# Performance work log

Measured on AMD Instinct MI355X. Metric: run time of the kernel, lower is better.

## Reference

```python
import jax, jax.numpy as jnp
import numpy as np

N_HEAD = 16


def setup_inputs() -> dict:
    B, T, C, H = 64, 128, 2048, N_HEAD
    hd = C // H
    key = jax.random.key(0)
    ks = jax.random.split(key, 5)
    x = jax.random.normal(ks[0], (B, T, C), dtype=jnp.float32)
    wq = jax.random.normal(ks[1], (C, C), dtype=jnp.float32) * 0.02
    wk = jax.random.normal(ks[2], (C, C), dtype=jnp.float32) * 0.02
    wv = jax.random.normal(ks[3], (C, C), dtype=jnp.float32) * 0.02
    wo = jax.random.normal(ks[4], (C, C), dtype=jnp.float32) * 0.02
    # RoPE frequencies: freqs_cis = exp(i * pos * theta_j), theta_j = 10000^(-2j/hd)
    pos = jnp.arange(T, dtype=jnp.float32)
    inv_freq = 1.0 / (10000.0 ** (jnp.arange(0, hd, 2, dtype=jnp.float32) / hd))  # [hd/2]
    ang = pos[:, None] * inv_freq[None, :]  # [T, hd/2]
    return {
        "x": x,
        "freqs_cos": jnp.cos(ang),
        "freqs_sin": jnp.sin(ang),
        "wq": wq, "wk": wk, "wv": wv, "wo": wo,
    }


def _apply_rope(t, cos, sin):
    # t: [B,T,H,hd]; complex multiply on interleaved (even, odd) pairs
    B, T, H, hd = t.shape
    tr = t.reshape(B, T, H, hd // 2, 2)
    te, to = tr[..., 0], tr[..., 1]
    c = cos[None, :, None, :]  # [1,T,1,hd/2]
    s = sin[None, :, None, :]
    oe = te * c - to * s
    oo = te * s + to * c
    return jnp.stack([oe, oo], axis=-1).reshape(B, T, H, hd)


def reference(x, freqs_cos, freqs_sin, wq, wk, wv, wo):
    B, T, C = x.shape
    H = N_HEAD
    hd = C // H
    q = (x @ wq.T).reshape(B, T, H, hd)
    k = (x @ wk.T).reshape(B, T, H, hd)
    v = (x @ wv.T).reshape(B, T, H, hd)
    q = _apply_rope(q, freqs_cos, freqs_sin)
    k = _apply_rope(k, freqs_cos, freqs_sin)
    # scores: [B,H,T,S]
    scores = jnp.einsum("bthd,bshd->bhts", q, k) / (hd ** 0.5)
    causal = jnp.tril(jnp.ones((T, T), dtype=bool))
    scores = jnp.where(causal[None, None], scores, jnp.float32(-jnp.inf))
    probs = jax.nn.softmax(scores, axis=-1)  # dropout is identity in eval
    out = jnp.einsum("bhts,bshd->bthd", probs, v).reshape(B, T, C)
    return out @ wo.T
```

## Files before the change

kernel.cpp:

```cpp
#include <hip/hip_runtime.h>
#include <cstdint>


typedef unsigned short ushort;
typedef __bf16 bf16x8 __attribute__((ext_vector_type(8)));
typedef float floatx4 __attribute__((ext_vector_type(4)));

__device__ __forceinline__ ushort f2bf(float f) {
  union { float f; uint32_t u; } v; v.f = f;
  uint32_t r = v.u + 0x7FFFu + ((v.u >> 16) & 1u);
  return (ushort)(r >> 16);
}
__device__ __forceinline__ float bf2f(ushort h) {
  union { uint32_t u; float f; } v; v.u = ((uint32_t)h) << 16;
  return v.f;
}

__device__ __forceinline__ void load_lds16(const void* g, void* l) {
  __builtin_amdgcn_global_load_lds(
      (__attribute__((address_space(1))) void*)(uintptr_t)g,
      (__attribute__((address_space(3))) void*)(uint32_t)(uintptr_t)l,
      16, 0, 0);
}

__device__ __forceinline__ void store_out(ushort* C, size_t i, float v) { C[i] = f2bf(v); }
__device__ __forceinline__ void store_out(float* C, size_t i, float v) { C[i] = v; }

template <typename OutT>
__device__ __forceinline__ void gemm_bt_body(const ushort* __restrict__ A,
                                             const ushort* __restrict__ B,
                                             OutT* __restrict__ C,
                                             int M, int N, int K) {
  __shared__ __align__(16) ushort As[128 * 32];
  __shared__ __align__(16) ushort Bs[128 * 32];
  const int tid = threadIdx.x;
  const int wave = tid >> 6, lane = tid & 63;
  const int quad = lane >> 4, colv = lane & 15;
  const int m0 = blockIdx.x * 128, n0 = blockIdx.y * 128;
  const int wm = (wave & 1) * 64, wn = (wave >> 1) * 64;

  floatx4 acc[4][4] = {};

  const int row0 = tid >> 2;
  const int gsw = (tid & 3) ^ ((row0 >> 1) & 3);
  const int c0 = gsw * 8;

  int aoff[4], boff[4];
#pragma unroll
  for (int i = 0; i < 4; ++i) {
    int ra = wm + i * 16 + colv;
    aoff[i] = ra * 32 + ((quad ^ ((ra >> 1) & 3)) << 3);
    int rb = wn + i * 16 + colv;
    boff[i] = rb * 32 + ((quad ^ ((rb >> 1) & 3)) << 3);
  }

  for (int k0 = 0; k0 < K; k0 += 32) {
    if (k0) __syncthreads();
    const ushort* Ab = A + (size_t)(m0 + row0) * K + k0 + c0;
    const ushort* Bb = B + (size_t)(n0 + row0) * K + k0 + c0;
    load_lds16(Ab, &As[wave * 512]);
    load_lds16(Bb, &Bs[wave * 512]);
    load_lds16(Ab + (size_t)64 * K, &As[wave * 512 + 2048]);
    load_lds16(Bb + (size_t)64 * K, &Bs[wave * 512 + 2048]);
    __syncthreads();

    bf16x8 af[4], bfr[4];
#pragma unroll
    for (int i = 0; i < 4; ++i) af[i] = *(const bf16x8*)&As[aoff[i]];
#pragma unroll
    for (int j = 0; j < 4; ++j) bfr[j] = *(const bf16x8*)&Bs[boff[j]];
#pragma unroll
    for (int i = 0; i < 4; ++i)
#pragma unroll
      for (int j = 0; j < 4; ++j)
        acc[i][j] = __builtin_amdgcn_mfma_f32_16x16x32_bf16(af[i], bfr[j], acc[i][j], 0, 0, 0);
  }

#pragma unroll
  for (int i = 0; i < 4; ++i)
#pragma unroll
    for (int j = 0; j < 4; ++j)
#pragma unroll
      for (int r = 0; r < 4; ++r) {
        int m = m0 + wm + i * 16 + quad * 4 + r;
        int n = n0 + wn + j * 16 + colv;
        store_out(C, (size_t)m * N + n, acc[i][j][r]);
      }
}

__global__ __launch_bounds__(256) void gemm_qkv(
    const ushort* __restrict__ A, const ushort* __restrict__ Wq,
    const ushort* __restrict__ Wk, const ushort* __restrict__ Wv,
    ushort* __restrict__ Q, ushort* __restrict__ Kb, ushort* __restrict__ V) {
  const ushort* B = (blockIdx.z == 0) ? Wq : (blockIdx.z == 1) ? Wk : Wv;
  ushort* C = (blockIdx.z == 0) ? Q : (blockIdx.z == 1) ? Kb : V;
  gemm_bt_body<ushort>(A, B, C, 8192, 2048, 2048);
}

__global__ __launch_bounds__(256) void gemm_out_k(
    const ushort* __restrict__ A, const ushort* __restrict__ B,
    float* __restrict__ C) {
  gemm_bt_body<float>(A, B, C, 8192, 2048, 2048);
}

#define NX 4194304u
#define NW 1048576u
__global__ void cvt_all(const float* __restrict__ x, const float* __restrict__ wq,
                        const float* __restrict__ wk, const float* __restrict__ wv,
                        const float* __restrict__ wo,
                        ushort* __restrict__ xb, ushort* __restrict__ wqb,
                        ushort* __restrict__ wkb, ushort* __restrict__ wvb,
                        ushort* __restrict__ wob) {
  uint32_t i = blockIdx.x * 256u + threadIdx.x;
  const float* src;
  ushort* dst;
  uint32_t off;
  if (i < NX) {
    src = x; dst = xb; off = i;
  } else {
    uint32_t i2 = i - NX;
    uint32_t r = i2 >> 20;
    off = i2 & (NW - 1u);
    src = (r == 0) ? wq : (r == 1) ? wk : (r == 2) ? wv : wo;
    dst = (r == 0) ? wqb : (r == 1) ? wkb : (r == 2) ? wvb : wob;
  }
  float4 v = ((const float4*)src)[off];
  ushort4 o;
  o.x = f2bf(v.x); o.y = f2bf(v.y); o.z = f2bf(v.z); o.w = f2bf(v.w);
  ((ushort4*)dst)[off] = o;
}

__global__ __launch_bounds__(256) void attn_kernel(
    const ushort* __restrict__ Q, const ushort* __restrict__ K,
    const ushort* __restrict__ V, const float* __restrict__ Cf,
    const float* __restrict__ Sf, ushort* __restrict__ O) {
  __shared__ __align__(16) ushort Qs[128 * 128];
  __shared__ __align__(16) ushort KVs[128 * 128];
  const int b = blockIdx.x >> 4, h = blockIdx.x & 15;
  const int tid = threadIdx.x, wave = tid >> 6, lane = tid & 63;
  const int quad = lane >> 4, colv = lane & 15;
  const size_t gbase = (size_t)b * 262144 + (size_t)h * 128;

#pragma unroll
  for (int sgi = 0; sgi < 8; ++sgi) {
    int seg = tid + sgi * 256;
    int t = seg >> 4, g = seg & 15;
    uint4 qv = *(const uint4*)(Q + gbase + (size_t)t * 2048 + g * 8);
    uint4 kv = *(const uint4*)(K + gbase + (size_t)t * 2048 + g * 8);
    float4 cf = *(const float4*)(Cf + t * 64 + g * 4);
    float4 sf = *(const float4*)(Sf + t * 64 + g * 4);
    uint32_t* qw = (uint32_t*)&qv;
    uint32_t* kw = (uint32_t*)&kv;
#pragma unroll
    for (int j = 0; j < 4; ++j) {
      float c = (&cf.x)[j], s = (&sf.x)[j];
      uint32_t w = qw[j];
      float e = bf2f((ushort)(w & 0xFFFF)), o = bf2f((ushort)(w >> 16));
      qw[j] = (uint32_t)f2bf(e * c - o * s) | ((uint32_t)f2bf(e * s + o * c) << 16);
      w = kw[j];
      e = bf2f((ushort)(w & 0xFFFF)); o = bf2f((ushort)(w >> 16));
      kw[j] = (uint32_t)f2bf(e * c - o * s) | ((uint32_t)f2bf(e * s + o * c) << 16);
    }
    int so = t * 128 + ((g ^ (t & 15)) << 3);
    *(uint4*)&Qs[so] = qv;
    *(uint4*)&KVs[so] = kv;
  }
  __syncthreads();

  floatx4 accs[2][8] = {};
#pragma unroll
  for (int kc = 0; kc < 4; ++kc) {
    bf16x8 af[2], bfr[8];
#pragma unroll
    for (int i = 0; i < 2; ++i) {
      int r = wave * 32 + i * 16 + colv;
      af[i] = *(const bf16x8*)&Qs[r * 128 + ((((kc << 2) | quad) ^ (r & 15)) << 3)];
    }
#pragma unroll
    for (int j = 0; j < 8; ++j) {
      int r = j * 16 + colv;
      bfr[j] = *(const bf16x8*)&KVs[r * 128 + ((((kc << 2) | quad) ^ (r & 15)) << 3)];
    }
#pragma unroll
    for (int i = 0; i < 2; ++i)
#pragma unroll
      for (int j = 0; j < 8; ++j)
        accs[i][j] = __builtin_amdgcn_mfma_f32_16x16x32_bf16(af[i], bfr[j], accs[i][j], 0, 0, 0);
  }

  const float scale = 0.08838834764831845f;
#pragma unroll
  for (int i = 0; i < 2; ++i)
#pragma unroll
    for (int r = 0; r < 4; ++r) {
      int t = wave * 32 + i * 16 + quad * 4 + r;
      float mx = -1e30f;
#pragma unroll
      for (int j = 0; j < 8; ++j) {
        int s = j * 16 + colv;
        float v = accs[i][j][r] * scale;
        v = (s <= t) ? v : -1e30f;
        accs[i][j][r] = v;
        mx = fmaxf(mx, v);
      }
#pragma unroll
      for (int off = 1; off < 16; off <<= 1) mx = fmaxf(mx, __shfl_xor(mx, off, 64));
      float l = 0.f;
#pragma unroll
      for (int j = 0; j < 8; ++j) {
        float p = __expf(accs[i][j][r] - mx);
        accs[i][j][r] = p;
        l += p;
      }
#pragma unroll
      for (int off = 1; off < 16; off <<= 1) l += __shfl_xor(l, off, 64);
      float inv = 1.0f / l;
#pragma unroll
      for (int j = 0; j < 8; ++j) {
        int s = j * 16 + colv;
        Qs[t * 128 + ((((s >> 3) ^ (t & 15)) << 3) | (s & 7))] = f2bf(accs[i][j][r] * inv);
      }
    }
  __syncthreads();

#pragma unroll
  for (int sgi = 0; sgi < 8; ++sgi) {
    int seg = tid + sgi * 256;
    int t = seg >> 4;
    int dg = (seg & 15) << 3;
    uint4 vv = *(const uint4*)(V + gbase + (size_t)t * 2048 + dg);
    const ushort* vp = (const ushort*)&vv;
#pragma unroll
    for (int jj = 0; jj < 8; ++jj) {
      int d = dg + jj;
      KVs[d * 128 + ((((t >> 3) ^ (d & 15)) << 3) | (t & 7))] = vp[jj];
    }
  }
  __syncthreads();

  floatx4 acco[2][8] = {};
#pragma unroll
  for (int kc = 0; kc < 4; ++kc) {
    bf16x8 af[2], bfr[8];
#pragma unroll
    for (int i = 0; i < 2; ++i) {
      int r = wave * 32 + i * 16 + colv;
      af[i] = *(const bf16x8*)&Qs[r * 128 + ((((kc << 2) | quad) ^ (r & 15)) << 3)];
    }
#pragma unroll
    for (int j = 0; j < 8; ++j) {
      int r = j * 16 + colv;
      bfr[j] = *(const bf16x8*)&KVs[r * 128 + ((((kc << 2) | quad) ^ (r & 15)) << 3)];
    }
#pragma unroll
    for (int i = 0; i < 2; ++i)
#pragma unroll
      for (int j = 0; j < 8; ++j)
        acco[i][j] = __builtin_amdgcn_mfma_f32_16x16x32_bf16(af[i], bfr[j], acco[i][j], 0, 0, 0);
  }

#pragma unroll
  for (int i = 0; i < 2; ++i)
#pragma unroll
    for (int j = 0; j < 8; ++j)
#pragma unroll
      for (int r = 0; r < 4; ++r) {
        int t = wave * 32 + i * 16 + quad * 4 + r;
        int d = j * 16 + colv;
        O[gbase + (size_t)t * 2048 + d] = f2bf(acco[i][j][r]);
      }
}

extern "C" void kernel_launch(void* const* d_in, const int* in_sizes, int n_in,
                              void* d_out, int out_size, void* d_ws, size_t ws_size,
                              hipStream_t stream) {
  const float* x    = (const float*)d_in[0];
  const float* fcos = (const float*)d_in[1];
  const float* fsin = (const float*)d_in[2];
  const float* wq   = (const float*)d_in[3];
  const float* wk   = (const float*)d_in[4];
  const float* wv   = (const float*)d_in[5];
  const float* wo   = (const float*)d_in[6];
  float* out = (float*)d_out;

  const size_t CC = 2048ull * 2048ull;
  const size_t MC = 8192ull * 2048ull;
  ushort* wob = (ushort*)d_ws;
  ushort* xb  = wob + CC;
  ushort* wqb = xb + MC;
  ushort* wkb = wqb + CC;
  ushort* wvb = wkb + CC;
  ushort* Qb  = wvb + CC;
  ushort* Kb  = Qb + MC;
  ushort* Vb  = Kb + MC;

  unsigned cvt_blocks = (unsigned)((MC + 4 * CC) / 4 / 256);
  cvt_all<<<dim3(cvt_blocks), 256, 0, stream>>>(x, wq, wk, wv, wo, xb, wqb, wkb, wvb, wob);

  gemm_qkv<<<dim3(64, 16, 3), 256, 0, stream>>>(xb, wqb, wkb, wvb, Qb, Kb, Vb);
  attn_kernel<<<dim3(1024), 256, 0, stream>>>(Qb, Kb, Vb, fcos, fsin, xb);
  gemm_out_k<<<dim3(64, 16), 256, 0, stream>>>(xb, wob, out);
}
```

Measured before the change: 524.0 us.

## Rewrite GEMMs as 256x256-tile double-buffered pipelined kernels with 8 waves

Both projection GEMMs switch from 128x128 tiles with K-step 32 and a single LDS buffer to 256x256 tiles with K-step 64, double-buffered LDS and 512 threads. Global-to-LDS loads for later K tiles are interleaved with the MFMA phases, using explicit barriers, vmcnt waits and s_setprio. The aim is to hide memory latency and raise arithmetic intensity per block. In exchange it uses 128KB of LDS and far more accumulator registers per block, and the grid shrinks to 768 and 256 blocks, which may leave CUs underfilled and risks sync bugs.

```diff
diff --git a/kernel.cpp b/kernel.cpp
--- a/kernel.cpp
+++ b/kernel.cpp
@@ -26,81 +26,160 @@
 __device__ __forceinline__ void store_out(ushort* C, size_t i, float v) { C[i] = f2bf(v); }
 __device__ __forceinline__ void store_out(float* C, size_t i, float v) { C[i] = v; }
 
+__device__ __forceinline__ void phase_mid() {
+  __builtin_amdgcn_s_barrier();
+  asm volatile("s_waitcnt lgkmcnt(0)" ::: "memory");
+  __builtin_amdgcn_sched_barrier(0);
+}
+__device__ __forceinline__ void phase_end() {
+  __builtin_amdgcn_s_barrier();
+  __builtin_amdgcn_sched_barrier(0);
+}
+
 template <typename OutT>
-__device__ __forceinline__ void gemm_bt_body(const ushort* __restrict__ A,
+__device__ __forceinline__ void gemm256_body(const ushort* __restrict__ A,
                                              const ushort* __restrict__ B,
                                              OutT* __restrict__ C,
                                              int M, int N, int K) {
-  __shared__ __align__(16) ushort As[128 * 32];
-  __shared__ __align__(16) ushort Bs[128 * 32];
+  (void)M;
+  __shared__ __align__(16) ushort As[2][256 * 64];
+  __shared__ __align__(16) ushort Bs[2][256 * 64];
   const int tid = threadIdx.x;
   const int wave = tid >> 6, lane = tid & 63;
   const int quad = lane >> 4, colv = lane & 15;
-  const int m0 = blockIdx.x * 128, n0 = blockIdx.y * 128;
-  const int wm = (wave & 1) * 64, wn = (wave >> 1) * 64;
-
-  floatx4 acc[4][4] = {};
-
-  const int row0 = tid >> 2;
-  const int gsw = (tid & 3) ^ ((row0 >> 1) & 3);
-  const int c0 = gsw * 8;
-
-  int aoff[4], boff[4];
-#pragma unroll
-  for (int i = 0; i < 4; ++i) {
-    int ra = wm + i * 16 + colv;
-    aoff[i] = ra * 32 + ((quad ^ ((ra >> 1) & 3)) << 3);
-    int rb = wn + i * 16 + colv;
-    boff[i] = rb * 32 + ((quad ^ ((rb >> 1) & 3)) << 3);
-  }
-
-  for (int k0 = 0; k0 < K; k0 += 32) {
-    if (k0) __syncthreads();
-    const ushort* Ab = A + (size_t)(m0 + row0) * K + k0 + c0;
-    const ushort* Bb = B + (size_t)(n0 + row0) * K + k0 + c0;
-    load_lds16(Ab, &As[wave * 512]);
-    load_lds16(Bb, &Bs[wave * 512]);
-    load_lds16(Ab + (size_t)64 * K, &As[wave * 512 + 2048]);
-    load_lds16(Bb + (size_t)64 * K, &Bs[wave * 512 + 2048]);
-    __syncthreads();
-
-    bf16x8 af[4], bfr[4];
-#pragma unroll
-    for (int i = 0; i < 4; ++i) af[i] = *(const bf16x8*)&As[aoff[i]];
-#pragma unroll
-    for (int j = 0; j < 4; ++j) bfr[j] = *(const bf16x8*)&Bs[boff[j]];
-#pragma unroll
-    for (int i = 0; i < 4; ++i)
-#pragma unroll
-      for (int j = 0; j < 4; ++j)
-        acc[i][j] = __builtin_amdgcn_mfma_f32_16x16x32_bf16(af[i], bfr[j], acc[i][j], 0, 0, 0);
-  }
-
-#pragma unroll
-  for (int i = 0; i < 4; ++i)
-#pragma unroll
-    for (int j = 0; j < 4; ++j)
+  const int wm = wave & 1, wn = wave >> 1;
+  const int m0 = blockIdx.x * 256, n0 = blockIdx.y * 256;
+
+  const int a_base = (wm * 128 + colv) * 64;
+  const int b_base = (wn * 64 + colv) * 64;
+  const int kg0 = ((quad) ^ (colv & 7)) << 3;
+  const int kg1 = ((quad | 4) ^ (colv & 7)) << 3;
+
+  const int srow = tid >> 3;
+  const int scol = ((tid & 7) ^ (srow & 7)) << 3;
+  const ushort* Ag = A + (size_t)(m0 + srow) * K + scol;
+  const ushort* Bg = B + (size_t)(n0 + srow) * K + scol;
+  const int ldsw = wave * 512;
+
+  floatx4 acc[8][4] = {};
+  bf16x8 af[4][2], bfr[4][2];
+
+#define STAGE(Gb, T, half, kt)                                             \
+  {                                                                        \
+    const ushort* g_ = (Gb) + (size_t)((half) * 128) * K + (kt) * 64;      \
+    load_lds16(g_, &(T)[(half) * 8192 + ldsw]);                            \
+    load_lds16(g_ + (size_t)64 * K, &(T)[(half) * 8192 + 4096 + ldsw]);    \
+  }
+
+#define READ_B_ALL(bi)                                                     \
+  _Pragma("unroll") for (int nf = 0; nf < 4; ++nf) {                       \
+    bfr[nf][0] = *(const bf16x8*)&Bs[bi][b_base + nf * 1024 + kg0];        \
+    bfr[nf][1] = *(const bf16x8*)&Bs[bi][b_base + nf * 1024 + kg1];        \
+  }
+
+#define READ_A(bi, off)                                                    \
+  _Pragma("unroll") for (int mf = 0; mf < 4; ++mf) {                       \
+    af[mf][0] = *(const bf16x8*)&As[bi][a_base + (off) + mf * 1024 + kg0]; \
+    af[mf][1] = *(const bf16x8*)&As[bi][a_base + (off) + mf * 1024 + kg1]; \
+  }
+
+#define MFMA16(ks, mo)                                                     \
+  __builtin_amdgcn_s_setprio(1);                                           \
+  _Pragma("unroll") for (int mf = 0; mf < 4; ++mf)                         \
+  _Pragma("unroll") for (int nf = 0; nf < 4; ++nf)                         \
+    acc[(mo) + mf][nf] = __builtin_amdgcn_mfma_f32_16x16x32_bf16(          \
+        af[mf][(ks)], bfr[nf][(ks)], acc[(mo) + mf][nf], 0, 0, 0);         \
+  __builtin_amdgcn_s_setprio(0);
+
+  STAGE(Bg, Bs[0], 0, 0)
+  STAGE(Bg, Bs[0], 1, 0)
+  STAGE(Ag, As[0], 0, 0)
+  STAGE(Ag, As[0], 1, 0)
+  STAGE(Bg, Bs[1], 0, 1)
+  STAGE(Bg, Bs[1], 1, 1)
+  STAGE(Ag, As[1], 0, 1)
+  asm volatile("s_waitcnt vmcnt(6)" ::: "memory");
+  __builtin_amdgcn_s_barrier();
+  __builtin_amdgcn_sched_barrier(0);
+
+  const int NT = K >> 6;
+#pragma unroll 1
+  for (int it = 0; it < (NT >> 1); ++it) {
+    const int s0 = (2 * it + 2 < NT) ? 2 * it + 2 : NT - 1;
+    const int s1 = (2 * it + 3 < NT) ? 2 * it + 3 : NT - 1;
+
+    READ_B_ALL(0)
+    READ_A(0, 0)
+    STAGE(Ag, As[1], 1, 2 * it + 1)
+    phase_mid();
+    MFMA16(0, 0)
+    phase_end();
+    STAGE(Bg, Bs[0], 0, s0)
+    phase_mid();
+    MFMA16(1, 0)
+    phase_end();
+    READ_A(0, 4096)
+    STAGE(Bg, Bs[0], 1, s0)
+    phase_mid();
+    MFMA16(0, 4)
+    phase_end();
+    STAGE(Ag, As[0], 0, s0)
+    asm volatile("s_waitcnt vmcnt(6)" ::: "memory");
+    phase_mid();
+    MFMA16(1, 4)
+    phase_end();
+    READ_B_ALL(1)
+    READ_A(1, 0)
+    STAGE(Ag, As[0], 1, s0)
+    phase_mid();
+    MFMA16(0, 0)
+    phase_end();
+    STAGE(Bg, Bs[1], 0, s1)
+    phase_mid();
+    MFMA16(1, 0)
+    phase_end();
+    READ_A(1, 4096)
+    STAGE(Bg, Bs[1], 1, s1)
+    phase_mid();
+    MFMA16(0, 4)
+    phase_end();
+    STAGE(Ag, As[1], 0, s1)
+    asm volatile("s_waitcnt vmcnt(6)" ::: "memory");
+    phase_mid();
+    MFMA16(1, 4)
+    phase_end();
+  }
+  asm volatile("s_waitcnt vmcnt(0)" ::: "memory");
+
+#pragma unroll
+  for (int mf = 0; mf < 8; ++mf)
+#pragma unroll
+    for (int nf = 0; nf < 4; ++nf)
 #pragma unroll
       for (int r = 0; r < 4; ++r) {
-        int m = m0 + wm + i * 16 + quad * 4 + r;
-        int n = n0 + wn + j * 16 + colv;
-        store_out(C, (size_t)m * N + n, acc[i][j][r]);
-      }
-}
-
-__global__ __launch_bounds__(256) void gemm_qkv(
+        int m = m0 + wm * 128 + mf * 16 + quad * 4 + r;
+        int n = n0 + wn * 64 + nf * 16 + colv;
+        store_out(C, (size_t)m * N + n, acc[mf][nf][r]);
+      }
+#undef STAGE
+#undef READ_B_ALL
+#undef READ_A
+#undef MFMA16
+}
+
+__global__ __launch_bounds__(512) void gemm_qkv(
     const ushort* __restrict__ A, const ushort* __restrict__ Wq,
     const ushort* __restrict__ Wk, const ushort* __restrict__ Wv,
     ushort* __restrict__ Q, ushort* __restrict__ Kb, ushort* __restrict__ V) {
   const ushort* B = (blockIdx.z == 0) ? Wq : (blockIdx.z == 1) ? Wk : Wv;
   ushort* C = (blockIdx.z == 0) ? Q : (blockIdx.z == 1) ? Kb : V;
-  gemm_bt_body<ushort>(A, B, C, 8192, 2048, 2048);
-}
-
-__global__ __launch_bounds__(256) void gemm_out_k(
+  gemm256_body<ushort>(A, B, C, 8192, 2048, 2048);
+}
+
+__global__ __launch_bounds__(512) void gemm_out_k(
     const ushort* __restrict__ A, const ushort* __restrict__ B,
     float* __restrict__ C) {
-  gemm_bt_body<float>(A, B, C, 8192, 2048, 2048);
+  gemm256_body<float>(A, B, C, 8192, 2048, 2048);
 }
 
 #define NX 4194304u
@@ -297,7 +376,7 @@
   unsigned cvt_blocks = (unsigned)((MC + 4 * CC) / 4 / 256);
   cvt_all<<<dim3(cvt_blocks), 256, 0, stream>>>(x, wq, wk, wv, wo, xb, wqb, wkb, wvb, wob);
 
-  gemm_qkv<<<dim3(64, 16, 3), 256, 0, stream>>>(xb, wqb, wkb, wvb, Qb, Kb, Vb);
+  gemm_qkv<<<dim3(32, 8, 3), 512, 0, stream>>>(xb, wqb, wkb, wvb, Qb, Kb, Vb);
   attn_kernel<<<dim3(1024), 256, 0, stream>>>(Qb, Kb, Vb, fcos, fsin, xb);
-  gemm_out_k<<<dim3(64, 16), 256, 0, stream>>>(xb, wob, out);
-}
+  gemm_out_k<<<dim3(32, 8), 512, 0, stream>>>(xb, wob, out);
+}
```

Result: faster. 448.2 us (-14.5%).
